# Optimization experiments

Measured on AMD Instinct MI355X. Metric: run time of the kernel, lower is better.

The kernel has to match this reference:

```python
import jax, jax.numpy as jnp
import numpy as np

NUM_HEADS = 12


def setup_inputs() -> dict:
    key = jax.random.key(0)
    k1, k2, k3 = jax.random.split(key, 3)
    B, F, P, D = 8, 16, 196, 768
    x = jax.random.normal(k1, (B, F, P, D), dtype=jnp.float32)
    w_qkv = jax.random.normal(k2, (3 * D, D), dtype=jnp.float32) * (D ** -0.5)
    w_proj = jax.random.normal(k3, (D, D), dtype=jnp.float32) * (D ** -0.5)
    b_proj = jnp.zeros((D,), dtype=jnp.float32)
    return {"x": x, "w_qkv": w_qkv, "w_proj": w_proj, "b_proj": b_proj}


def reference(x, w_qkv, w_proj, b_proj):
    B, F, P, D = x.shape
    H = NUM_HEADS
    hd = D // H
    H2 = H // 2
    scale = hd ** -0.5
    N = F * P

    xf = x.reshape(B, N, D)
    qkv = jnp.einsum('bnd,ed->bne', xf, w_qkv)              # (B, N, 3D)
    qkv = qkv.reshape(B, N, 3, H, hd).transpose(2, 0, 3, 1, 4)
    q, k, v = qkv[0], qkv[1], qkv[2]                         # (B, H, N, hd)

    # split heads: first half spatial, second half temporal
    qs, qt = q[:, :H2], q[:, H2:]
    ks, kt = k[:, :H2], k[:, H2:]
    vs, vt = v[:, :H2], v[:, H2:]

    # spatial attention over patches within each frame
    qs = qs.reshape(B * F, H2, P, hd)
    ks = ks.reshape(B * F, H2, P, hd)
    vs = vs.reshape(B * F, H2, P, hd)
    attn_s = jax.nn.softmax(jnp.einsum('nhqd,nhkd->nhqk', qs, ks) * scale, axis=-1)
    ws = jnp.einsum('nhqk,nhkd->nhqd', attn_s, vs)           # (B*F, H2, P, hd)

    # temporal attention: raw row-major reshape, faithful to torch .reshape
    qt = qt.reshape(B * P, H2, F, hd)
    kt = kt.reshape(B * P, H2, F, hd)
    vt = vt.reshape(B * P, H2, F, hd)
    attn_t = jax.nn.softmax(jnp.einsum('mhqd,mhkd->mhqk', qt, kt) * scale, axis=-1)
    wt = jnp.einsum('mhqk,mhkd->mhqd', attn_t, vt)           # (B*P, H2, F, hd)

    ws = ws.reshape(B, H2, N, hd)
    wt = wt.reshape(B, H2, N, hd)
    w = jnp.concatenate([ws, wt], axis=1)                    # (B, H, N, hd)
    w = w.transpose(0, 2, 1, 3).reshape(B, N, D)

    out = jnp.einsum('bnd,ed->bne', w, w_proj) + b_proj
    return out.reshape(B, F, P, D)
```

## Files before the change

kernel.cpp:

```cpp
#include <hip/hip_runtime.h>

#define DEV __device__ __forceinline__

typedef _Float16 half8  __attribute__((ext_vector_type(8)));
typedef _Float16 half4h __attribute__((ext_vector_type(4)));
typedef float    f32x4  __attribute__((ext_vector_type(4)));

static constexpr int Bb = 8;
static constexpr int Ff = 16;
static constexpr int Pp = 196;
static constexpr int Dd = 768;
static constexpr int Hh = 12;
static constexpr int HD = 64;
static constexpr int Nn = 3136;
static constexpr int NC = 392;

#define MFMA(a, b, c) __builtin_amdgcn_mfma_f32_16x16x32_f16(a, b, c, 0, 0, 0)

DEV void gll16(const _Float16* g, _Float16* l) {
  __builtin_amdgcn_global_load_lds(
      (__attribute__((address_space(1))) void*)(g),
      (__attribute__((address_space(3))) void*)(l), 16, 0, 0);
}

DEV void lds_fence() { asm volatile("s_waitcnt lgkmcnt(0)" ::: "memory"); }

__global__ __launch_bounds__(256) void cvt_all(const float* __restrict__ x,
                                               const float* __restrict__ wq,
                                               const float* __restrict__ wp,
                                               _Float16* __restrict__ xh,
                                               _Float16* __restrict__ wqh,
                                               _Float16* __restrict__ wph) {
  const int NX = 4816896, NQ = 442368;
  int i = blockIdx.x * 256 + threadIdx.x;
  const float* s;
  _Float16* d;
  int j;
  if (i < NX) { s = x; d = xh; j = i; }
  else if (i < NX + NQ) { s = wq; d = wqh; j = i - NX; }
  else { s = wp; d = wph; j = i - NX - NQ; }
  f32x4 v = ((const f32x4*)s)[j];
  half4h h;
  h.x = (_Float16)v.x; h.y = (_Float16)v.y;
  h.z = (_Float16)v.z; h.w = (_Float16)v.w;
  ((half4h*)d)[j] = h;
}

__global__ __launch_bounds__(256) void gemm_qkv(const _Float16* __restrict__ X,
                                                const _Float16* __restrict__ W,
                                                _Float16* __restrict__ Q8,
                                                _Float16* __restrict__ K8,
                                                _Float16* __restrict__ V8) {
  __shared__ __align__(16) _Float16 smem[128 * 132];
  _Float16* As = smem;
  _Float16* Bs = smem + 128 * 32;
  const int tid = threadIdx.x;
  const int lane = tid & 63, wid = tid >> 6;
  const int l15 = lane & 15, quad = lane >> 4;
  const int row0 = blockIdx.y * 128;
  const int e0 = blockIdx.x * 128;
  const int wm = (wid >> 1) * 64, wn = (wid & 1) * 64;

  const _Float16* Ag = X + (size_t)row0 * Dd;
  const _Float16* Bg = W + (size_t)e0 * Dd;

  f32x4 acc[4][4];
#pragma unroll
  for (int i = 0; i < 4; ++i)
#pragma unroll
    for (int j = 0; j < 4; ++j) acc[i][j] = (f32x4)0.0f;

  const int c0 = tid, c1 = tid + 256;
  const int r0s = c0 >> 2, o0 = ((c0 & 3) ^ ((r0s >> 1) & 3)) * 8;
  const int r1s = c1 >> 2, o1 = ((c1 & 3) ^ ((r1s >> 1) & 3)) * 8;
  const int csel = ((quad ^ ((l15 >> 1) & 3))) * 8;

  for (int kt = 0; kt < 24; ++kt) {
    const int k0 = kt * 32;
    __syncthreads();
    gll16(Ag + (size_t)r0s * Dd + k0 + o0, As + c0 * 8);
    gll16(Bg + (size_t)r0s * Dd + k0 + o0, Bs + c0 * 8);
    gll16(Ag + (size_t)r1s * Dd + k0 + o1, As + c1 * 8);
    gll16(Bg + (size_t)r1s * Dd + k0 + o1, Bs + c1 * 8);
    __syncthreads();
    half8 af[4], bf[4];
#pragma unroll
    for (int t = 0; t < 4; ++t) {
      af[t] = *(const half8*)(As + (wm + t * 16 + l15) * 32 + csel);
      bf[t] = *(const half8*)(Bs + (wn + t * 16 + l15) * 32 + csel);
    }
#pragma unroll
    for (int i = 0; i < 4; ++i)
#pragma unroll
      for (int j = 0; j < 4; ++j) acc[i][j] = MFMA(af[i], bf[j], acc[i][j]);
  }

  __syncthreads();
  const int tsel = e0 / Dd;
  if (tsel == 2) {
#pragma unroll
    for (int i = 0; i < 4; ++i)
#pragma unroll
      for (int j = 0; j < 4; ++j) {
        const int m = wm + i * 16 + quad * 4;
        const int n = wn + j * 16 + l15;
        half4h hv;
        hv.x = (_Float16)acc[i][j].x; hv.y = (_Float16)acc[i][j].y;
        hv.z = (_Float16)acc[i][j].z; hv.w = (_Float16)acc[i][j].w;
        *(half4h*)(smem + n * 132 + m) = hv;
      }
    __syncthreads();
    for (int c = tid; c < 2048; c += 256) {
      const int ncl = c >> 7, el = c & 127;
      const int e = e0 + el;
      const int h = (e >> 6) % Hh, d = e & 63;
      const int r = row0 + ncl * 8;
      const int b = r / Nn, n = r % Nn;
      const half4h lo = *(const half4h*)(smem + el * 132 + ncl * 8);
      const half4h hi = *(const half4h*)(smem + el * 132 + ncl * 8 + 4);
      half8 v;
#pragma unroll
      for (int z = 0; z < 4; ++z) { v[z] = lo[z]; v[4 + z] = hi[z]; }
      *(half8*)(V8 + (((size_t)(b * Hh + h) * NC + (n >> 3)) * 64 + d) * 8) = v;
    }
  } else {
    _Float16* Ob = (tsel == 0) ? Q8 : K8;
#pragma unroll
    for (int i = 0; i < 4; ++i)
#pragma unroll
      for (int j = 0; j < 4; ++j) {
        const int n = wn + j * 16 + l15;
#pragma unroll
        for (int r = 0; r < 4; ++r) {
          const int m = wm + i * 16 + quad * 4 + r;
          smem[m * 132 + n] = (_Float16)acc[i][j][r];
        }
      }
    __syncthreads();
    for (int c = tid; c < 2048; c += 256) {
      const int ec = c >> 7, m = c & 127;
      const int r = row0 + m;
      const int b = r / Nn, n = r % Nn;
      const int e = e0 + ec * 8;
      const int h = (e >> 6) % Hh, dc = (e >> 3) & 7;
      const half4h lo = *(const half4h*)(smem + m * 132 + ec * 8);
      const half4h hi = *(const half4h*)(smem + m * 132 + ec * 8 + 4);
      half8 v;
#pragma unroll
      for (int z = 0; z < 4; ++z) { v[z] = lo[z]; v[4 + z] = hi[z]; }
      *(half8*)(Ob + (((size_t)(b * Hh + h) * 8 + dc) * Nn + n) * 8) = v;
    }
  }
}

__global__ __launch_bounds__(256) void gemm_proj(const _Float16* __restrict__ Wbuf,
                                                 const _Float16* __restrict__ Wp,
                                                 const float* __restrict__ bias,
                                                 float* __restrict__ Out) {
  __shared__ __align__(16) _Float16 smem[128 * 64];
  _Float16* As = smem;
  _Float16* Bs = smem + 128 * 32;
  const int tid = threadIdx.x;
  const int lane = tid & 63, wid = tid >> 6;
  const int l15 = lane & 15, quad = lane >> 4;
  const int row0 = blockIdx.y * 128;
  const int e0 = blockIdx.x * 128;
  const int wm = (wid >> 1) * 64, wn = (wid & 1) * 64;

  const _Float16* Ag = Wbuf + (size_t)row0 * Dd;
  const _Float16* Bg = Wp + (size_t)e0 * Dd;

  f32x4 acc[4][4];
#pragma unroll
  for (int i = 0; i < 4; ++i)
#pragma unroll
    for (int j = 0; j < 4; ++j) acc[i][j] = (f32x4)0.0f;

  const int c0 = tid, c1 = tid + 256;
  const int r0s = c0 >> 2, o0 = ((c0 & 3) ^ ((r0s >> 1) & 3)) * 8;
  const int r1s = c1 >> 2, o1 = ((c1 & 3) ^ ((r1s >> 1) & 3)) * 8;
  const int csel = ((quad ^ ((l15 >> 1) & 3))) * 8;

  for (int kt = 0; kt < 24; ++kt) {
    const int k0 = kt * 32;
    __syncthreads();
    gll16(Ag + (size_t)r0s * Dd + k0 + o0, As + c0 * 8);
    gll16(Bg + (size_t)r0s * Dd + k0 + o0, Bs + c0 * 8);
    gll16(Ag + (size_t)r1s * Dd + k0 + o1, As + c1 * 8);
    gll16(Bg + (size_t)r1s * Dd + k0 + o1, Bs + c1 * 8);
    __syncthreads();
    half8 af[4], bf[4];
#pragma unroll
    for (int t = 0; t < 4; ++t) {
      af[t] = *(const half8*)(As + (wm + t * 16 + l15) * 32 + csel);
      bf[t] = *(const half8*)(Bs + (wn + t * 16 + l15) * 32 + csel);
    }
#pragma unroll
    for (int i = 0; i < 4; ++i)
#pragma unroll
      for (int j = 0; j < 4; ++j) acc[i][j] = MFMA(af[i], bf[j], acc[i][j]);
  }

#pragma unroll
  for (int j = 0; j < 4; ++j) {
    const int e = e0 + wn + j * 16 + l15;
    const float bj = bias[e];
#pragma unroll
    for (int i = 0; i < 4; ++i) {
      const int rb = row0 + wm + i * 16 + quad * 4;
#pragma unroll
      for (int r = 0; r < 4; ++r)
        Out[(size_t)(rb + r) * Dd + e] = acc[i][j][r] + bj;
    }
  }
}

__global__ __launch_bounds__(256) void attn_spatial(const _Float16* __restrict__ Q8,
                                                    const _Float16* __restrict__ K8,
                                                    const _Float16* __restrict__ V8,
                                                    _Float16* __restrict__ Wbuf) {
  __shared__ __align__(16) _Float16 Vs[64 * 216];
  __shared__ __align__(16) _Float16 Plds[4][16 * 232];
  const int tid = threadIdx.x;
  const int lane = tid & 63, wid = tid >> 6;
  const int l15 = lane & 15, quad = lane >> 4;
  const int gid = blockIdx.x;
  const int h = gid % 6, f = (gid / 6) % Ff, b = gid / 96;
  const size_t bh = (size_t)b * Hh + h;
  const int g0 = f * Pp;
  const int off = g0 & 7;
  const int nc0 = g0 >> 3;
  const _Float16* Qp = Q8 + bh * 8 * (size_t)Nn * 8;
  const _Float16* Kp = K8 + bh * 8 * (size_t)Nn * 8;

  for (int c = tid; c < 26 * 64; c += 256) {
    const int d = c & 63, ncl = c >> 6;
    const half8 v = *(const half8*)(V8 + ((bh * NC + nc0 + ncl) * 64 + d) * 8);
    _Float16* dst = Vs + d * 216 + (8 - off) + ncl * 8;
    half4h lo, hi;
#pragma unroll
    for (int z = 0; z < 4; ++z) { lo[z] = v[z]; hi[z] = v[4 + z]; }
    *(half4h*)dst = lo;
    *(half4h*)(dst + 4) = hi;
  }
  _Float16* Pw = &Plds[wid][0];
  if (quad < 3) {
    half8 z8;
#pragma unroll
    for (int z = 0; z < 8; ++z) z8[z] = (_Float16)0.0f;
    *(half8*)(Pw + l15 * 232 + 208 + quad * 8) = z8;
  }
  __syncthreads();

  half8 h8z;
#pragma unroll
  for (int z = 0; z < 8; ++z) h8z[z] = (_Float16)0.0f;

  for (int it = 0; it < 4; ++it) {
    const int qi = wid + it * 4;
    if (qi > 12) continue;
    const int qr = qi * 16 + l15;
    const int qtok = g0 + (qr < 195 ? qr : 195);
    const half8 bq0 = *(const half8*)(Qp + ((size_t)quad * Nn + qtok) * 8);
    const half8 bq1 = *(const half8*)(Qp + ((size_t)(quad + 4) * Nn + qtok) * 8);

    f32x4 ex[13];
    float rs = 0.0f;
#pragma unroll
    for (int kt = 0; kt < 13; ++kt) {
      const int krr = kt * 16 + l15;
      const int ktok = g0 + (krr < 195 ? krr : 195);
      const half8 ak0 = *(const half8*)(Kp + ((size_t)quad * Nn + ktok) * 8);
      const half8 ak1 = *(const half8*)(Kp + ((size_t)(quad + 4) * Nn + ktok) * 8);
      f32x4 t = (f32x4)0.0f;
      t = MFMA(ak0, bq0, t);
      t = MFMA(ak1, bq1, t);
      f32x4 e;
#pragma unroll
      for (int r = 0; r < 4; ++r) e[r] = __expf(t[r] * 0.125f);
      if (kt == 12 && quad >= 1) e = (f32x4)0.0f;
      ex[kt] = e;
      rs += e[0] + e[1] + e[2] + e[3];
    }
#pragma unroll
    for (int kt = 0; kt < 13; ++kt)
#pragma unroll
      for (int r = 0; r < 4; ++r)
        Pw[l15 * 232 + kt * 16 + quad * 4 + r] = (_Float16)ex[kt][r];
    rs += __shfl_xor(rs, 16);
    rs += __shfl_xor(rs, 32);
    lds_fence();

    f32x4 acc[4];
#pragma unroll
    for (int mt = 0; mt < 4; ++mt) acc[mt] = (f32x4)0.0f;
#pragma unroll
    for (int c = 0; c < 7; ++c) {
      const half8 bp = *(const half8*)(Pw + l15 * 232 + c * 32 + quad * 8);
      const int k0 = c * 32 + quad * 8;
#pragma unroll
      for (int mt = 0; mt < 4; ++mt) {
        const int d = mt * 16 + l15;
        half8 av = h8z;
        if (k0 < 196) av = *(const half8*)(Vs + d * 216 + 8 + k0);
        acc[mt] = MFMA(av, bp, acc[mt]);
      }
    }
    const float inv = 1.0f / rs;
    if (qr < 196) {
      _Float16* base = Wbuf + (size_t)(b * Nn + g0 + qr) * Dd + h * HD;
#pragma unroll
      for (int mt = 0; mt < 4; ++mt) {
        half4h o;
#pragma unroll
        for (int r = 0; r < 4; ++r) o[r] = (_Float16)(acc[mt][r] * inv);
        *(half4h*)(base + mt * 16 + quad * 4) = o;
      }
    }
    __builtin_amdgcn_sched_barrier(0);
  }
}

__global__ __launch_bounds__(256) void attn_temporal(const _Float16* __restrict__ Q8,
                                                     const _Float16* __restrict__ K8,
                                                     const _Float16* __restrict__ V8,
                                                     _Float16* __restrict__ Wbuf) {
  __shared__ __align__(16) _Float16 Plds[4][16 * 40];
  const int tid = threadIdx.x;
  const int lane = tid & 63, wid = tid >> 6;
  const int l15 = lane & 15, quad = lane >> 4;
  const int p = blockIdx.x * 4 + wid;
  const int J0 = p << 4;
  const int b = J0 / 18816;
  const int rem = J0 % 18816;
  const int hh = rem / Nn;
  const int n0 = rem % Nn;
  const size_t bh = (size_t)b * Hh + 6 + hh;
  const _Float16* Qp = Q8 + bh * 8 * (size_t)Nn * 8;
  const _Float16* Kp = K8 + bh * 8 * (size_t)Nn * 8;
  _Float16* Pw = &Plds[wid][0];

  const int tok = n0 + l15;
  const half8 bq0 = *(const half8*)(Qp + ((size_t)quad * Nn + tok) * 8);
  const half8 bq1 = *(const half8*)(Qp + ((size_t)(quad + 4) * Nn + tok) * 8);
  const half8 ak0 = *(const half8*)(Kp + ((size_t)quad * Nn + tok) * 8);
  const half8 ak1 = *(const half8*)(Kp + ((size_t)(quad + 4) * Nn + tok) * 8);
  f32x4 t = (f32x4)0.0f;
  t = MFMA(ak0, bq0, t);
  t = MFMA(ak1, bq1, t);
  f32x4 e;
#pragma unroll
  for (int r = 0; r < 4; ++r) e[r] = __expf(t[r] * 0.125f);
  float rs = e[0] + e[1] + e[2] + e[3];
  rs += __shfl_xor(rs, 16);
  rs += __shfl_xor(rs, 32);

#pragma unroll
  for (int r = 0; r < 4; ++r) Pw[l15 * 40 + quad * 4 + r] = (_Float16)e[r];
  {
    half4h z4;
    z4.x = z4.y = z4.z = z4.w = (_Float16)0.0f;
    *(half4h*)(Pw + l15 * 40 + 16 + quad * 4) = z4;
  }
  lds_fence();

  const half8 bp = *(const half8*)(Pw + l15 * 40 + quad * 8);
  half8 h8z;
#pragma unroll
  for (int z = 0; z < 8; ++z) h8z[z] = (_Float16)0.0f;

  const float inv = 1.0f / rs;
  _Float16* base = Wbuf + (size_t)(b * Nn + n0 + l15) * Dd + (6 + hh) * HD;
#pragma unroll
  for (int mt = 0; mt < 4; ++mt) {
    const int d = mt * 16 + l15;
    half8 av = h8z;
    if (quad < 2)
      av = *(const half8*)(V8 + ((bh * NC + (n0 >> 3) + quad) * 64 + d) * 8);
    f32x4 acc = (f32x4)0.0f;
    acc = MFMA(av, bp, acc);
    half4h o;
#pragma unroll
    for (int r = 0; r < 4; ++r) o[r] = (_Float16)(acc[r] * inv);
    *(half4h*)(base + mt * 16 + quad * 4) = o;
  }
}

extern "C" void kernel_launch(void* const* d_in, const int* in_sizes, int n_in,
                              void* d_out, int out_size, void* d_ws, size_t ws_size,
                              hipStream_t stream) {
  const float* x = (const float*)d_in[0];
  const float* w_qkv = (const float*)d_in[1];
  const float* w_proj = (const float*)d_in[2];
  const float* b_proj = (const float*)d_in[3];
  float* out = (float*)d_out;

  _Float16* Xh = (_Float16*)d_ws;
  _Float16* Q8 = Xh + 19267584;
  _Float16* K8 = Q8 + 19267584;
  _Float16* V8 = K8 + 19267584;
  _Float16* Wqh = V8 + 19267584;
  _Float16* Wph = Wqh + 1769472;

  cvt_all<<<21120, 256, 0, stream>>>(x, w_qkv, w_proj, Xh, Wqh, Wph);
  gemm_qkv<<<dim3(18, 196), 256, 0, stream>>>(Xh, Wqh, Q8, K8, V8);
  attn_spatial<<<768, 256, 0, stream>>>(Q8, K8, V8, Xh);
  attn_temporal<<<2352, 256, 0, stream>>>(Q8, K8, V8, Xh);
  gemm_proj<<<dim3(6, 196), 256, 0, stream>>>(Xh, Wph, b_proj, out);
}
```

Baseline: 369.4 us.

## Double GEMM K-tile to 64, split QKV GEMM into three launches, fold softmax scale into Q

Both GEMMs now stage a 64-wide K slice per iteration with an 8-way XOR swizzle, halving the number of barrier pairs and main-loop iterations. The QKV projection is split into three launches (Q, K, V), each with an explicit mode argument instead of deriving the output from the block column. The 1/8 attention scale is applied when Q is written in fp16, so the attention kernels drop the per-score multiply. Serial launches of the three QKV GEMMs may lose some concurrency, and pre-scaling Q changes fp16 rounding slightly.

```diff
diff --git a/kernel.cpp b/kernel.cpp
--- a/kernel.cpp
+++ b/kernel.cpp
@@ -50,10 +50,11 @@
                                                 const _Float16* __restrict__ W,
                                                 _Float16* __restrict__ Q8,
                                                 _Float16* __restrict__ K8,
-                                                _Float16* __restrict__ V8) {
+                                                _Float16* __restrict__ V8,
+                                                const int mode) {
   __shared__ __align__(16) _Float16 smem[128 * 132];
   _Float16* As = smem;
-  _Float16* Bs = smem + 128 * 32;
+  _Float16* Bs = smem + 128 * 64;
   const int tid = threadIdx.x;
   const int lane = tid & 63, wid = tid >> 6;
   const int l15 = lane & 15, quad = lane >> 4;
@@ -70,34 +71,41 @@
 #pragma unroll
     for (int j = 0; j < 4; ++j) acc[i][j] = (f32x4)0.0f;
 
-  const int c0 = tid, c1 = tid + 256;
-  const int r0s = c0 >> 2, o0 = ((c0 & 3) ^ ((r0s >> 1) & 3)) * 8;
-  const int r1s = c1 >> 2, o1 = ((c1 & 3) ^ ((r1s >> 1) & 3)) * 8;
-  const int csel = ((quad ^ ((l15 >> 1) & 3))) * 8;
-
-  for (int kt = 0; kt < 24; ++kt) {
-    const int k0 = kt * 32;
-    __syncthreads();
-    gll16(Ag + (size_t)r0s * Dd + k0 + o0, As + c0 * 8);
-    gll16(Bg + (size_t)r0s * Dd + k0 + o0, Bs + c0 * 8);
-    gll16(Ag + (size_t)r1s * Dd + k0 + o1, As + c1 * 8);
-    gll16(Bg + (size_t)r1s * Dd + k0 + o1, Bs + c1 * 8);
-    __syncthreads();
-    half8 af[4], bf[4];
-#pragma unroll
-    for (int t = 0; t < 4; ++t) {
-      af[t] = *(const half8*)(As + (wm + t * 16 + l15) * 32 + csel);
-      bf[t] = *(const half8*)(Bs + (wn + t * 16 + l15) * 32 + csel);
-    }
-#pragma unroll
-    for (int i = 0; i < 4; ++i)
-#pragma unroll
-      for (int j = 0; j < 4; ++j) acc[i][j] = MFMA(af[i], bf[j], acc[i][j]);
+  int srow[4], soff[4];
+#pragma unroll
+  for (int i = 0; i < 4; ++i) {
+    const int slot = i * 256 + tid;
+    srow[i] = slot >> 3;
+    soff[i] = ((slot & 7) ^ (srow[i] & 7)) * 8;
+  }
+
+  for (int kt = 0; kt < 12; ++kt) {
+    const int k0 = kt * 64;
+    __syncthreads();
+#pragma unroll
+    for (int i = 0; i < 4; ++i) {
+      gll16(Ag + (size_t)srow[i] * Dd + k0 + soff[i], As + (i * 256 + tid) * 8);
+      gll16(Bg + (size_t)srow[i] * Dd + k0 + soff[i], Bs + (i * 256 + tid) * 8);
+    }
+    __syncthreads();
+#pragma unroll
+    for (int kh = 0; kh < 2; ++kh) {
+      half8 af[4], bf[4];
+      const int sc = ((kh * 4 + quad) ^ (l15 & 7)) * 8;
+#pragma unroll
+      for (int t = 0; t < 4; ++t) {
+        af[t] = *(const half8*)(As + (wm + t * 16 + l15) * 64 + sc);
+        bf[t] = *(const half8*)(Bs + (wn + t * 16 + l15) * 64 + sc);
+      }
+#pragma unroll
+      for (int i = 0; i < 4; ++i)
+#pragma unroll
+        for (int j = 0; j < 4; ++j) acc[i][j] = MFMA(af[i], bf[j], acc[i][j]);
+    }
   }
 
   __syncthreads();
-  const int tsel = e0 / Dd;
-  if (tsel == 2) {
+  if (mode == 2) {
 #pragma unroll
     for (int i = 0; i < 4; ++i)
 #pragma unroll
@@ -113,7 +121,7 @@
     for (int c = tid; c < 2048; c += 256) {
       const int ncl = c >> 7, el = c & 127;
       const int e = e0 + el;
-      const int h = (e >> 6) % Hh, d = e & 63;
+      const int h = e >> 6, d = e & 63;
       const int r = row0 + ncl * 8;
       const int b = r / Nn, n = r % Nn;
       const half4h lo = *(const half4h*)(smem + el * 132 + ncl * 8);
@@ -124,7 +132,8 @@
       *(half8*)(V8 + (((size_t)(b * Hh + h) * NC + (n >> 3)) * 64 + d) * 8) = v;
     }
   } else {
-    _Float16* Ob = (tsel == 0) ? Q8 : K8;
+    _Float16* Ob = (mode == 0) ? Q8 : K8;
+    const float qs = (mode == 0) ? 0.125f : 1.0f;
 #pragma unroll
     for (int i = 0; i < 4; ++i)
 #pragma unroll
@@ -133,7 +142,7 @@
 #pragma unroll
         for (int r = 0; r < 4; ++r) {
           const int m = wm + i * 16 + quad * 4 + r;
-          smem[m * 132 + n] = (_Float16)acc[i][j][r];
+          smem[m * 132 + n] = (_Float16)(acc[i][j][r] * qs);
         }
       }
     __syncthreads();
@@ -142,7 +151,7 @@
       const int r = row0 + m;
       const int b = r / Nn, n = r % Nn;
       const int e = e0 + ec * 8;
-      const int h = (e >> 6) % Hh, dc = (e >> 3) & 7;
+      const int h = e >> 6, dc = (e >> 3) & 7;
       const half4h lo = *(const half4h*)(smem + m * 132 + ec * 8);
       const half4h hi = *(const half4h*)(smem + m * 132 + ec * 8 + 4);
       half8 v;
@@ -157,9 +166,9 @@
                                                  const _Float16* __restrict__ Wp,
                                                  const float* __restrict__ bias,
                                                  float* __restrict__ Out) {
-  __shared__ __align__(16) _Float16 smem[128 * 64];
+  __shared__ __align__(16) _Float16 smem[128 * 128];
   _Float16* As = smem;
-  _Float16* Bs = smem + 128 * 32;
+  _Float16* Bs = smem + 128 * 64;
   const int tid = threadIdx.x;
   const int lane = tid & 63, wid = tid >> 6;
   const int l15 = lane & 15, quad = lane >> 4;
@@ -176,29 +185,37 @@
 #pragma unroll
     for (int j = 0; j < 4; ++j) acc[i][j] = (f32x4)0.0f;
 
-  const int c0 = tid, c1 = tid + 256;
-  const int r0s = c0 >> 2, o0 = ((c0 & 3) ^ ((r0s >> 1) & 3)) * 8;
-  const int r1s = c1 >> 2, o1 = ((c1 & 3) ^ ((r1s >> 1) & 3)) * 8;
-  const int csel = ((quad ^ ((l15 >> 1) & 3))) * 8;
-
-  for (int kt = 0; kt < 24; ++kt) {
-    const int k0 = kt * 32;
-    __syncthreads();
-    gll16(Ag + (size_t)r0s * Dd + k0 + o0, As + c0 * 8);
-    gll16(Bg + (size_t)r0s * Dd + k0 + o0, Bs + c0 * 8);
-    gll16(Ag + (size_t)r1s * Dd + k0 + o1, As + c1 * 8);
-    gll16(Bg + (size_t)r1s * Dd + k0 + o1, Bs + c1 * 8);
-    __syncthreads();
-    half8 af[4], bf[4];
-#pragma unroll
-    for (int t = 0; t < 4; ++t) {
-      af[t] = *(const half8*)(As + (wm + t * 16 + l15) * 32 + csel);
-      bf[t] = *(const half8*)(Bs + (wn + t * 16 + l15) * 32 + csel);
-    }
-#pragma unroll
-    for (int i = 0; i < 4; ++i)
-#pragma unroll
-      for (int j = 0; j < 4; ++j) acc[i][j] = MFMA(af[i], bf[j], acc[i][j]);
+  int srow[4], soff[4];
+#pragma unroll
+  for (int i = 0; i < 4; ++i) {
+    const int slot = i * 256 + tid;
+    srow[i] = slot >> 3;
+    soff[i] = ((slot & 7) ^ (srow[i] & 7)) * 8;
+  }
+
+  for (int kt = 0; kt < 12; ++kt) {
+    const int k0 = kt * 64;
+    __syncthreads();
+#pragma unroll
+    for (int i = 0; i < 4; ++i) {
+      gll16(Ag + (size_t)srow[i] * Dd + k0 + soff[i], As + (i * 256 + tid) * 8);
+      gll16(Bg + (size_t)srow[i] * Dd + k0 + soff[i], Bs + (i * 256 + tid) * 8);
+    }
+    __syncthreads();
+#pragma unroll
+    for (int kh = 0; kh < 2; ++kh) {
+      half8 af[4], bf[4];
+      const int sc = ((kh * 4 + quad) ^ (l15 & 7)) * 8;
+#pragma unroll
+      for (int t = 0; t < 4; ++t) {
+        af[t] = *(const half8*)(As + (wm + t * 16 + l15) * 64 + sc);
+        bf[t] = *(const half8*)(Bs + (wn + t * 16 + l15) * 64 + sc);
+      }
+#pragma unroll
+      for (int i = 0; i < 4; ++i)
+#pragma unroll
+        for (int j = 0; j < 4; ++j) acc[i][j] = MFMA(af[i], bf[j], acc[i][j]);
+    }
   }
 
 #pragma unroll
@@ -277,7 +294,7 @@
       t = MFMA(ak1, bq1, t);
       f32x4 e;
 #pragma unroll
-      for (int r = 0; r < 4; ++r) e[r] = __expf(t[r] * 0.125f);
+      for (int r = 0; r < 4; ++r) e[r] = __expf(t[r]);
       if (kt == 12 && quad >= 1) e = (f32x4)0.0f;
       ex[kt] = e;
       rs += e[0] + e[1] + e[2] + e[3];
@@ -350,7 +367,7 @@
   t = MFMA(ak1, bq1, t);
   f32x4 e;
 #pragma unroll
-  for (int r = 0; r < 4; ++r) e[r] = __expf(t[r] * 0.125f);
+  for (int r = 0; r < 4; ++r) e[r] = __expf(t[r]);
   float rs = e[0] + e[1] + e[2] + e[3];
   rs += __shfl_xor(rs, 16);
   rs += __shfl_xor(rs, 32);
@@ -403,7 +420,9 @@
   _Float16* Wph = Wqh + 1769472;
 
   cvt_all<<<21120, 256, 0, stream>>>(x, w_qkv, w_proj, Xh, Wqh, Wph);
-  gemm_qkv<<<dim3(18, 196), 256, 0, stream>>>(Xh, Wqh, Q8, K8, V8);
+  gemm_qkv<<<dim3(6, 196), 256, 0, stream>>>(Xh, Wqh,             Q8, K8, V8, 0);
+  gemm_qkv<<<dim3(6, 196), 256, 0, stream>>>(Xh, Wqh + 768 * Dd,  Q8, K8, V8, 1);
+  gemm_qkv<<<dim3(6, 196), 256, 0, stream>>>(Xh, Wqh + 1536 * Dd, Q8, K8, V8, 2);
   attn_spatial<<<768, 256, 0, stream>>>(Q8, K8, V8, Xh);
   attn_temporal<<<2352, 256, 0, stream>>>(Q8, K8, V8, Xh);
   gemm_proj<<<dim3(6, 196), 256, 0, stream>>>(Xh, Wph, b_proj, out);
```

Measured after the change: 410.6 us. +11.1%, slower.
